# Kernel tuning notes

Measured on AMD Instinct MI355X. Metric: run time of the kernel, lower is better.

## Reference

```python
import jax, jax.numpy as jnp
import numpy as np

N, T, H, D, E, P, R = 50000, 16, 512, 256, 200000, 100000, 3
LN_EPS = 1e-5
BN_EPS = 1e-5


def setup_inputs() -> dict:
    key = jax.random.key(0)
    ks = jax.random.split(key, 32)
    ri = lambda k, shape, hi: jax.random.randint(k, shape, 0, hi)
    rn = lambda k, shape, scale=0.05: (jax.random.normal(k, shape, dtype=jnp.float32) * scale)
    return {
        "node_type_ids": ri(ks[0], (N,), T),
        "src0": ri(ks[1], (E,), N), "dst0": ri(ks[2], (E,), N),
        "src1": ri(ks[3], (E,), N), "dst1": ri(ks[4], (E,), N),
        "src2": ri(ks[5], (E,), N), "dst2": ri(ks[6], (E,), N),
        "pairs": ri(ks[7], (2, P), N),
        "degrees": ri(ks[8], (N,), 100),
        "node_emb": rn(ks[9], (N, H)),
        "type_emb": rn(ks[10], (T, H)),
        "w_loop_in": rn(ks[11], (H, H)),
        "w_rel_in": rn(ks[12], (R, H, H)),
        "w_loop_res": rn(ks[13], (H, H)),
        "w_rel_res": rn(ks[14], (R, H, H)),
        "ln_g": jnp.ones((H,), jnp.float32),
        "ln_b": jnp.zeros((H,), jnp.float32),
        "w_loop_out": rn(ks[15], (H, D)),
        "w_rel_out": rn(ks[16], (R, H, D)),
        "lp_w1": rn(ks[17], (3 * D, D)),
        "lp_b1": jnp.zeros((D,), jnp.float32),
        "bn_g": jnp.ones((D,), jnp.float32),
        "bn_b": jnp.zeros((D,), jnp.float32),
        "bn_mean": jnp.zeros((D,), jnp.float32),
        "bn_var": jnp.ones((D,), jnp.float32),
        "lp_w2": rn(ks[18], (D, 1)),
        "lp_b2": jnp.zeros((1,), jnp.float32),
        "alpha": jnp.float32(0.1),
        "beta": jnp.float32(0.1),
    }


def _rgcn(x, loop_w, rel_w, srcs, dsts):
    # out = x @ W_loop + sum_r (A_r @ x) @ W_r ; A_r unweighted COO -> segment_sum
    out = x @ loop_w
    for r in range(R):
        msg = jax.ops.segment_sum(x[srcs[r]], dsts[r], num_segments=x.shape[0])
        out = out + msg @ rel_w[r]
    return out


def _layernorm(h, g, b):
    mu = h.mean(-1, keepdims=True)
    var = h.var(-1, keepdims=True)
    return (h - mu) * jax.lax.rsqrt(var + LN_EPS) * g + b


def reference(node_type_ids, src0, dst0, src1, dst1, src2, dst2, pairs, degrees,
              node_emb, type_emb, w_loop_in, w_rel_in, w_loop_res, w_rel_res,
              ln_g, ln_b, w_loop_out, w_rel_out, lp_w1, lp_b1, bn_g, bn_b,
              bn_mean, bn_var, lp_w2, lp_b2, alpha, beta):
    srcs = (src0, src1, src2)
    dsts = (dst0, dst1, dst2)
    # encode
    x = node_emb + type_emb[node_type_ids]          # [N, H]
    x = jax.nn.relu(_rgcn(x, w_loop_in, w_rel_in, srcs, dsts))
    h = _rgcn(x, w_loop_res, w_rel_res, srcs, dsts)
    h = jax.nn.relu(_layernorm(h, ln_g, ln_b))      # dropout p=0 -> identity
    x = x + h
    z = _rgcn(x, w_loop_out, w_rel_out, srcs, dsts)  # [N, D]
    # score
    src_z = z[pairs[0]]                              # [P, D]
    dst_z = z[pairs[1]]
    src_deg = jnp.clip(degrees[pairs[0]], 1).astype(jnp.float32)
    dst_deg = jnp.clip(degrees[pairs[1]], 1).astype(jnp.float32)
    feats = jnp.concatenate([src_z, dst_z, src_z * dst_z], axis=-1)  # [P, 3D]
    h1 = jax.nn.relu(feats @ lp_w1 + lp_b1)
    # BatchNorm1d in eval mode: running stats
    h1 = (h1 - bn_mean) * jax.lax.rsqrt(bn_var + BN_EPS) * bn_g + bn_b
    mlp_score = (h1 @ lp_w2 + lp_b2).squeeze(-1)     # [P]
    base = mlp_score - jax.nn.relu(alpha) * jnp.log(src_deg) - jax.nn.relu(beta) * jnp.log(dst_deg)
    return base / (jnp.sqrt(src_deg) * jnp.sqrt(dst_deg) + 1e-8)
```

## Files before the change

kernel.cpp:

```cpp
#include <hip/hip_runtime.h>

typedef __attribute__((ext_vector_type(8))) _Float16 half8;
typedef __attribute__((ext_vector_type(4))) _Float16 half4;
typedef __attribute__((ext_vector_type(4))) float f32x4;

__global__ void k_encode(const float* __restrict__ emb, const float* __restrict__ temb,
                         const int* __restrict__ tids, _Float16* __restrict__ x, int n) {
  int i = blockIdx.x * 256 + threadIdx.x;
  if (i >= n * 64) return;
  int node = i >> 6, c = (i & 63) << 3;
  const float* e = emb + (size_t)node * 512 + c;
  const float* t = temb + (size_t)tids[node] * 512 + c;
  float4 a0 = *(const float4*)e, a1 = *(const float4*)(e + 4);
  float4 b0 = *(const float4*)t, b1 = *(const float4*)(t + 4);
  half8 o;
  o[0] = (_Float16)(a0.x + b0.x); o[1] = (_Float16)(a0.y + b0.y);
  o[2] = (_Float16)(a0.z + b0.z); o[3] = (_Float16)(a0.w + b0.w);
  o[4] = (_Float16)(a1.x + b1.x); o[5] = (_Float16)(a1.y + b1.y);
  o[6] = (_Float16)(a1.z + b1.z); o[7] = (_Float16)(a1.w + b1.w);
  *(half8*)(x + (size_t)node * 512 + c) = o;
}

__global__ void k_zero(int* __restrict__ p, int n) {
  int i = blockIdx.x * 256 + threadIdx.x;
  if (i < n) p[i] = 0;
}

__global__ void k_hist(const int* __restrict__ d0, const int* __restrict__ d1,
                       const int* __restrict__ d2, int* __restrict__ counts, int E, int Np1) {
  int e = blockIdx.x * 256 + threadIdx.x;
  if (e >= E) return;
  int r = blockIdx.y;
  const int* d = (r == 0) ? d0 : ((r == 1) ? d1 : d2);
  atomicAdd(&counts[r * Np1 + d[e] + 1], 1);
}

__global__ void k_scan(const int* __restrict__ counts, int* __restrict__ rowp, int n) {
  __shared__ int wsum[16];
  int r = blockIdx.x;
  const int* c = counts + (size_t)r * n;
  int* o = rowp + (size_t)r * n;
  int lane = threadIdx.x & 63, w = threadIdx.x >> 6;
  int off = 0;
  for (int base = 0; base < n; base += 1024) {
    int i = base + threadIdx.x;
    int v = (i < n) ? c[i] : 0;
    int sc = v;
    #pragma unroll
    for (int d = 1; d < 64; d <<= 1) {
      int t = __shfl_up(sc, (unsigned)d);
      if (lane >= d) sc += t;
    }
    if (lane == 63) wsum[w] = sc;
    __syncthreads();
    int wo = 0, tot = 0;
    #pragma unroll
    for (int ww = 0; ww < 16; ++ww) {
      int s = wsum[ww];
      if (ww < w) wo += s;
      tot += s;
    }
    if (i < n) o[i] = sc + wo + off;
    off += tot;
    __syncthreads();
  }
}

__global__ void k_copy(const int* __restrict__ a, int* __restrict__ b, int n) {
  int i = blockIdx.x * 256 + threadIdx.x;
  if (i < n) b[i] = a[i];
}

__global__ void k_fill(const int* __restrict__ s0, const int* __restrict__ s1, const int* __restrict__ s2,
                       const int* __restrict__ d0, const int* __restrict__ d1, const int* __restrict__ d2,
                       int* __restrict__ cursor, int* __restrict__ col_src, int E, int Np1) {
  int e = blockIdx.x * 256 + threadIdx.x;
  if (e >= E) return;
  int r = blockIdx.y;
  const int* dp = (r == 0) ? d0 : ((r == 1) ? d1 : d2);
  const int* sp = (r == 0) ? s0 : ((r == 1) ? s1 : s2);
  int pos = atomicAdd(&cursor[r * Np1 + dp[e]], 1);
  if (pos >= 0 && pos < E) col_src[(size_t)r * E + pos] = sp[e];
}

__global__ void k_aggregate(const _Float16* __restrict__ x, _Float16* __restrict__ agg,
                            const int* __restrict__ rowp, const int* __restrict__ col_src,
                            int N, int E) {
  int wid = (blockIdx.x * 256 + threadIdx.x) >> 6;
  int lane = threadIdx.x & 63;
  if (wid >= 3 * N) return;
  int r = wid / N;
  int n = wid - r * N;
  int beg = rowp[r * (N + 1) + n], end = rowp[r * (N + 1) + n + 1];
  const int* cs = col_src + (size_t)r * E;
  float acc[8] = {0, 0, 0, 0, 0, 0, 0, 0};
  for (int e = beg; e < end; ++e) {
    int s = cs[e];
    half8 v = *(const half8*)(x + (size_t)s * 512 + lane * 8);
    #pragma unroll
    for (int j = 0; j < 8; ++j) acc[j] += (float)v[j];
  }
  half8 o;
  #pragma unroll
  for (int j = 0; j < 8; ++j) o[j] = (_Float16)acc[j];
  *(half8*)(agg + (size_t)n * 1536 + r * 512 + lane * 8) = o;
}

__global__ void k_transpose(const float* __restrict__ Bl, const float* __restrict__ Br,
                            _Float16* __restrict__ Bt, int No, int K) {
  __shared__ float tile[64][65];
  int k0 = blockIdx.x * 64, n0 = blockIdx.y * 64;
  int nl = threadIdx.x & 63, kb = threadIdx.x >> 6;
  #pragma unroll
  for (int i = 0; i < 16; ++i) {
    int kl = kb + i * 4;
    int krow = k0 + kl;
    float v = (krow < 512) ? Bl[(size_t)krow * No + n0 + nl]
                           : Br[(size_t)(krow - 512) * No + n0 + nl];
    tile[kl][nl] = v;
  }
  __syncthreads();
  int kl = threadIdx.x & 63, nb = threadIdx.x >> 6;
  #pragma unroll
  for (int i = 0; i < 16; ++i) {
    int n2 = nb + i * 4;
    Bt[(size_t)(n0 + n2) * K + k0 + kl] = (_Float16)tile[kl][n2];
  }
}

#define LSTR 40

__global__ __launch_bounds__(256) void k_gemm_rgcn(
    const _Float16* __restrict__ Ain, const _Float16* __restrict__ Aagg,
    const _Float16* __restrict__ Bt, _Float16* __restrict__ C,
    int M, int Ncols, int K, int relu) {
  __shared__ __align__(16) _Float16 As[128 * LSTR];
  __shared__ __align__(16) _Float16 Bs[128 * LSTR];
  int tid = threadIdx.x;
  int bm0 = blockIdx.x * 128, bn0 = blockIdx.y * 128;
  int lane = tid & 63, wv = tid >> 6;
  int wm = wv & 1, wn = wv >> 1;
  int l16 = lane & 15, quad = lane >> 4;
  int srow = tid >> 1, scs = (tid & 1) * 16;
  int agr = bm0 + srow; if (agr >= M) agr = M - 1;
  int bgn = bn0 + srow;

  f32x4 acc[4][4];
  #pragma unroll
  for (int i = 0; i < 4; ++i)
    #pragma unroll
    for (int j = 0; j < 4; ++j) acc[i][j] = (f32x4){0.f, 0.f, 0.f, 0.f};

  for (int k0 = 0; k0 < K; k0 += 32) {
    __syncthreads();
    {
      const _Float16* src = (k0 < 512)
          ? Ain + (size_t)agr * 512 + k0 + scs
          : Aagg + (size_t)agr * 1536 + (k0 - 512) + scs;
      *(uint4*)&As[srow * LSTR + scs] = *(const uint4*)src;
      *(uint4*)&As[srow * LSTR + scs + 8] = *(const uint4*)(src + 8);
    }
    {
      const _Float16* src = Bt + (size_t)bgn * K + k0 + scs;
      *(uint4*)&Bs[srow * LSTR + scs] = *(const uint4*)src;
      *(uint4*)&Bs[srow * LSTR + scs + 8] = *(const uint4*)(src + 8);
    }
    __syncthreads();
    half8 af[4], bf[4];
    #pragma unroll
    for (int i = 0; i < 4; ++i)
      af[i] = *(const half8*)&As[(wm * 64 + i * 16 + l16) * LSTR + quad * 8];
    #pragma unroll
    for (int j = 0; j < 4; ++j)
      bf[j] = *(const half8*)&Bs[(wn * 64 + j * 16 + l16) * LSTR + quad * 8];
    #pragma unroll
    for (int i = 0; i < 4; ++i)
      #pragma unroll
      for (int j = 0; j < 4; ++j)
        acc[i][j] = __builtin_amdgcn_mfma_f32_16x16x32_f16(af[i], bf[j], acc[i][j], 0, 0, 0);
  }

  #pragma unroll
  for (int i = 0; i < 4; ++i)
    #pragma unroll
    for (int j = 0; j < 4; ++j)
      #pragma unroll
      for (int rg = 0; rg < 4; ++rg) {
        int row = bm0 + wm * 64 + i * 16 + quad * 4 + rg;
        int col = bn0 + wn * 64 + j * 16 + l16;
        if (row < M) {
          float v = acc[i][j][rg];
          if (relu) v = fmaxf(v, 0.f);
          C[(size_t)row * Ncols + col] = (_Float16)v;
        }
      }
}

__global__ __launch_bounds__(256) void k_gemm_link(
    const _Float16* __restrict__ z, const int* __restrict__ pairs,
    const _Float16* __restrict__ Bt,
    const float* __restrict__ b1, const float* __restrict__ bng, const float* __restrict__ bnb,
    const float* __restrict__ bnm, const float* __restrict__ bnv,
    _Float16* __restrict__ h1, int P, int K) {
  __shared__ __align__(16) _Float16 As[128 * LSTR];
  __shared__ __align__(16) _Float16 Bs[128 * LSTR];
  int tid = threadIdx.x;
  int bm0 = blockIdx.x * 128, bn0 = blockIdx.y * 128;
  int lane = tid & 63, wv = tid >> 6;
  int wm = wv & 1, wn = wv >> 1;
  int l16 = lane & 15, quad = lane >> 4;
  int srow = tid >> 1, scs = (tid & 1) * 16;
  int p = bm0 + srow; if (p >= P) p = P - 1;
  int sp = pairs[p], dp = pairs[P + p];
  const _Float16* zs = z + (size_t)sp * 256;
  const _Float16* zd = z + (size_t)dp * 256;
  int bgn = bn0 + srow;

  f32x4 acc[4][4];
  #pragma unroll
  for (int i = 0; i < 4; ++i)
    #pragma unroll
    for (int j = 0; j < 4; ++j) acc[i][j] = (f32x4){0.f, 0.f, 0.f, 0.f};

  for (int k0 = 0; k0 < K; k0 += 32) {
    __syncthreads();
    int seg = k0 >> 8;
    int kk = (k0 & 255) + scs;
    __attribute__((aligned(16))) _Float16 tmp[16];
    if (seg == 0) {
      *(uint4*)tmp = *(const uint4*)(zs + kk);
      *(uint4*)(tmp + 8) = *(const uint4*)(zs + kk + 8);
    } else if (seg == 1) {
      *(uint4*)tmp = *(const uint4*)(zd + kk);
      *(uint4*)(tmp + 8) = *(const uint4*)(zd + kk + 8);
    } else {
      half8 u0 = *(const half8*)(zs + kk), u1 = *(const half8*)(zs + kk + 8);
      half8 v0 = *(const half8*)(zd + kk), v1 = *(const half8*)(zd + kk + 8);
      #pragma unroll
      for (int j = 0; j < 8; ++j) {
        tmp[j] = (_Float16)((float)u0[j] * (float)v0[j]);
        tmp[j + 8] = (_Float16)((float)u1[j] * (float)v1[j]);
      }
    }
    *(uint4*)&As[srow * LSTR + scs] = *(const uint4*)tmp;
    *(uint4*)&As[srow * LSTR + scs + 8] = *(const uint4*)(tmp + 8);
    {
      const _Float16* src = Bt + (size_t)bgn * K + k0 + scs;
      *(uint4*)&Bs[srow * LSTR + scs] = *(const uint4*)src;
      *(uint4*)&Bs[srow * LSTR + scs + 8] = *(const uint4*)(src + 8);
    }
    __syncthreads();
    half8 af[4], bf[4];
    #pragma unroll
    for (int i = 0; i < 4; ++i)
      af[i] = *(const half8*)&As[(wm * 64 + i * 16 + l16) * LSTR + quad * 8];
    #pragma unroll
    for (int j = 0; j < 4; ++j)
      bf[j] = *(const half8*)&Bs[(wn * 64 + j * 16 + l16) * LSTR + quad * 8];
    #pragma unroll
    for (int i = 0; i < 4; ++i)
      #pragma unroll
      for (int j = 0; j < 4; ++j)
        acc[i][j] = __builtin_amdgcn_mfma_f32_16x16x32_f16(af[i], bf[j], acc[i][j], 0, 0, 0);
  }

  #pragma unroll
  for (int i = 0; i < 4; ++i)
    #pragma unroll
    for (int j = 0; j < 4; ++j) {
      int col = bn0 + wn * 64 + j * 16 + l16;
      float bb1 = b1[col], m = bnm[col], rs = rsqrtf(bnv[col] + 1e-5f);
      float gg = bng[col], bb = bnb[col];
      #pragma unroll
      for (int rg = 0; rg < 4; ++rg) {
        int row = bm0 + wm * 64 + i * 16 + quad * 4 + rg;
        if (row < P) {
          float v = fmaxf(acc[i][j][rg] + bb1, 0.f);
          v = (v - m) * rs * gg + bb;
          h1[(size_t)row * 256 + col] = (_Float16)v;
        }
      }
    }
}

__global__ void k_ln_res(const _Float16* __restrict__ h, const _Float16* __restrict__ x1,
                         const float* __restrict__ g, const float* __restrict__ b,
                         _Float16* __restrict__ out, int N) {
  int wid = (blockIdx.x * 256 + threadIdx.x) >> 6;
  int lane = threadIdx.x & 63;
  if (wid >= N) return;
  int c = lane * 8;
  half8 hv = *(const half8*)(h + (size_t)wid * 512 + c);
  float hf[8];
  float s = 0.f, sq = 0.f;
  #pragma unroll
  for (int j = 0; j < 8; ++j) {
    hf[j] = (float)hv[j];
    s += hf[j];
    sq += hf[j] * hf[j];
  }
  #pragma unroll
  for (int off = 32; off; off >>= 1) {
    s += __shfl_down(s, (unsigned)off);
    sq += __shfl_down(sq, (unsigned)off);
  }
  s = __shfl(s, 0); sq = __shfl(sq, 0);
  float mu = s * (1.f / 512.f);
  float var = sq * (1.f / 512.f) - mu * mu;
  float rs = rsqrtf(var + 1e-5f);
  float4 g0 = *(const float4*)(g + c), g1 = *(const float4*)(g + c + 4);
  float4 b0 = *(const float4*)(b + c), b1 = *(const float4*)(b + c + 4);
  float gf[8] = {g0.x, g0.y, g0.z, g0.w, g1.x, g1.y, g1.z, g1.w};
  float bf[8] = {b0.x, b0.y, b0.z, b0.w, b1.x, b1.y, b1.z, b1.w};
  half8 xv = *(const half8*)(x1 + (size_t)wid * 512 + c);
  half8 o;
  #pragma unroll
  for (int j = 0; j < 8; ++j) {
    float xw = (float)xv[j];
    o[j] = (_Float16)(xw + fmaxf((hf[j] - mu) * rs * gf[j] + bf[j], 0.f));
  }
  *(half8*)(out + (size_t)wid * 512 + c) = o;
}

__global__ void k_score(const _Float16* __restrict__ h1, const float* __restrict__ w2,
                        const float* __restrict__ b2, const int* __restrict__ pairs,
                        const int* __restrict__ degrees, const float* __restrict__ alpha,
                        const float* __restrict__ beta, float* __restrict__ out, int P) {
  int wid = (blockIdx.x * 256 + threadIdx.x) >> 6;
  int lane = threadIdx.x & 63;
  if (wid >= P) return;
  int c = lane * 4;
  half4 hv = *(const half4*)(h1 + (size_t)wid * 256 + c);
  float4 wv = *(const float4*)(w2 + c);
  float s = (float)hv[0] * wv.x + (float)hv[1] * wv.y + (float)hv[2] * wv.z + (float)hv[3] * wv.w;
  #pragma unroll
  for (int off = 32; off; off >>= 1) s += __shfl_down(s, (unsigned)off);
  if (lane == 0) {
    int sp = pairs[wid], dp = pairs[P + wid];
    float sd = (float)max(degrees[sp], 1);
    float dd = (float)max(degrees[dp], 1);
    float base = s + b2[0] - fmaxf(alpha[0], 0.f) * logf(sd) - fmaxf(beta[0], 0.f) * logf(dd);
    out[wid] = base / (sqrtf(sd) * sqrtf(dd) + 1e-8f);
  }
}

extern "C" void kernel_launch(void* const* d_in, const int* in_sizes, int n_in,
                              void* d_out, int out_size, void* d_ws, size_t ws_size,
                              hipStream_t stream) {
  const int N = 50000, E = 200000, P = 100000;
  const int Np1 = N + 1;
  const int* node_type = (const int*)d_in[0];
  const int* src0 = (const int*)d_in[1]; const int* dst0 = (const int*)d_in[2];
  const int* src1 = (const int*)d_in[3]; const int* dst1 = (const int*)d_in[4];
  const int* src2 = (const int*)d_in[5]; const int* dst2 = (const int*)d_in[6];
  const int* pairs = (const int*)d_in[7];
  const int* degrees = (const int*)d_in[8];
  const float* node_emb = (const float*)d_in[9];
  const float* type_emb = (const float*)d_in[10];
  const float* w_loop_in = (const float*)d_in[11];
  const float* w_rel_in = (const float*)d_in[12];
  const float* w_loop_res = (const float*)d_in[13];
  const float* w_rel_res = (const float*)d_in[14];
  const float* ln_g = (const float*)d_in[15];
  const float* ln_b = (const float*)d_in[16];
  const float* w_loop_out = (const float*)d_in[17];
  const float* w_rel_out = (const float*)d_in[18];
  const float* lp_w1 = (const float*)d_in[19];
  const float* lp_b1 = (const float*)d_in[20];
  const float* bn_g = (const float*)d_in[21];
  const float* bn_b = (const float*)d_in[22];
  const float* bn_mean = (const float*)d_in[23];
  const float* bn_var = (const float*)d_in[24];
  const float* lp_w2 = (const float*)d_in[25];
  const float* lp_b2 = (const float*)d_in[26];
  const float* alpha = (const float*)d_in[27];
  const float* beta = (const float*)d_in[28];
  float* out = (float*)d_out;

  char* ws = (char*)d_ws;
  size_t off = 0;
  auto alloc = [&](size_t bytes) {
    void* p = ws + off;
    off = (off + bytes + 255) & ~(size_t)255;
    return p;
  };
  _Float16* xb0 = (_Float16*)alloc((size_t)N * 512 * 2);
  _Float16* xb1 = (_Float16*)alloc((size_t)N * 512 * 2);
  _Float16* agg = (_Float16*)alloc((size_t)N * 1536 * 2);
  _Float16* Bt = (_Float16*)alloc((size_t)512 * 2048 * 2);
  int* counts = (int*)alloc((size_t)3 * Np1 * 4);
  int* rowp = (int*)alloc((size_t)3 * Np1 * 4);
  int* cursor = (int*)alloc((size_t)3 * Np1 * 4);
  int* col_src = (int*)alloc((size_t)3 * E * 4);
  if (off > ws_size) return;

  _Float16* z = xb1;
  _Float16* h1 = agg;

  k_zero<<<(3 * Np1 + 255) / 256, 256, 0, stream>>>(counts, 3 * Np1);
  dim3 gE((E + 255) / 256, 3);
  k_hist<<<gE, 256, 0, stream>>>(dst0, dst1, dst2, counts, E, Np1);
  k_scan<<<3, 1024, 0, stream>>>(counts, rowp, Np1);
  k_copy<<<(3 * Np1 + 255) / 256, 256, 0, stream>>>(rowp, cursor, 3 * Np1);
  k_fill<<<gE, 256, 0, stream>>>(src0, src1, src2, dst0, dst1, dst2, cursor, col_src, E, Np1);

  k_encode<<<(N * 64 + 255) / 256, 256, 0, stream>>>(node_emb, type_emb, node_type, xb0, N);

  int aggBlocks = (3 * N + 3) / 4;
  dim3 g1((N + 127) / 128, 4);
  dim3 g3((N + 127) / 128, 2);

  k_aggregate<<<aggBlocks, 256, 0, stream>>>(xb0, agg, rowp, col_src, N, E);
  k_transpose<<<dim3(32, 8), 256, 0, stream>>>(w_loop_in, w_rel_in, Bt, 512, 2048);
  k_gemm_rgcn<<<g1, 256, 0, stream>>>(xb0, agg, Bt, xb1, N, 512, 2048, 1);

  k_aggregate<<<aggBlocks, 256, 0, stream>>>(xb1, agg, rowp, col_src, N, E);
  k_transpose<<<dim3(32, 8), 256, 0, stream>>>(w_loop_res, w_rel_res, Bt, 512, 2048);
  k_gemm_rgcn<<<g1, 256, 0, stream>>>(xb1, agg, Bt, xb0, N, 512, 2048, 0);

  k_ln_res<<<(N + 3) / 4, 256, 0, stream>>>(xb0, xb1, ln_g, ln_b, xb0, N);

  k_aggregate<<<aggBlocks, 256, 0, stream>>>(xb0, agg, rowp, col_src, N, E);
  k_transpose<<<dim3(32, 4), 256, 0, stream>>>(w_loop_out, w_rel_out, Bt, 256, 2048);
  k_gemm_rgcn<<<g3, 256, 0, stream>>>(xb0, agg, Bt, z, N, 256, 2048, 0);

  k_transpose<<<dim3(12, 4), 256, 0, stream>>>(lp_w1, lp_w1 + 512 * 256, Bt, 256, 768);
  dim3 gl((P + 127) / 128, 2);
  k_gemm_link<<<gl, 256, 0, stream>>>(z, pairs, Bt, lp_b1, bn_g, bn_b, bn_mean, bn_var, h1, P, 768);

  k_score<<<(P + 3) / 4, 256, 0, stream>>>(h1, lp_w2, lp_b2, pairs, degrees, alpha, beta, out, P);
}
```

Before: 1.294 ms.

## Use direct global-to-LDS loads in RGCN GEMM and swap grid axes

The RGCN GEMM now stages A and B tiles with global_load_lds 16-byte loads straight into LDS instead of going through registers. The LDS padding (stride 40) is dropped to a dense stride of 32 to match the per-wave contiguous layout those loads write. Separately, the grid axes of both GEMMs are swapped so consecutive blocks share the same A row-block across N tiles, which should improve L2 reuse of activations. The unpadded LDS layout may add bank conflicts on the fragment reads.

```diff
diff --git a/kernel.cpp b/kernel.cpp
--- a/kernel.cpp
+++ b/kernel.cpp
@@ -3,6 +3,11 @@
 typedef __attribute__((ext_vector_type(8))) _Float16 half8;
 typedef __attribute__((ext_vector_type(4))) _Float16 half4;
 typedef __attribute__((ext_vector_type(4))) float f32x4;
+
+static __device__ __forceinline__ void gload16(const void* g, void* l) {
+  __builtin_amdgcn_global_load_lds((const __attribute__((address_space(1))) void*)g,
+                                   (__attribute__((address_space(3))) void*)l, 16, 0, 0);
+}
 
 __global__ void k_encode(const float* __restrict__ emb, const float* __restrict__ temb,
                          const int* __restrict__ tids, _Float16* __restrict__ x, int n) {
@@ -128,22 +133,32 @@
   }
 }
 
-#define LSTR 40
-
 __global__ __launch_bounds__(256) void k_gemm_rgcn(
     const _Float16* __restrict__ Ain, const _Float16* __restrict__ Aagg,
     const _Float16* __restrict__ Bt, _Float16* __restrict__ C,
     int M, int Ncols, int K, int relu) {
-  __shared__ __align__(16) _Float16 As[128 * LSTR];
-  __shared__ __align__(16) _Float16 Bs[128 * LSTR];
+  __shared__ __align__(16) _Float16 As[128 * 32];
+  __shared__ __align__(16) _Float16 Bs[128 * 32];
   int tid = threadIdx.x;
-  int bm0 = blockIdx.x * 128, bn0 = blockIdx.y * 128;
+  int bn0 = blockIdx.x * 128, bm0 = blockIdx.y * 128;
   int lane = tid & 63, wv = tid >> 6;
   int wm = wv & 1, wn = wv >> 1;
   int l16 = lane & 15, quad = lane >> 4;
-  int srow = tid >> 1, scs = (tid & 1) * 16;
-  int agr = bm0 + srow; if (agr >= M) agr = M - 1;
-  int bgn = bn0 + srow;
+
+  int rl = wv * 16 + (lane >> 2);
+  int kq = (lane & 3) * 8;
+  int ra0 = bm0 + rl;       if (ra0 >= M) ra0 = M - 1;
+  int ra1 = bm0 + 64 + rl;  if (ra1 >= M) ra1 = M - 1;
+  int rb0 = bn0 + rl, rb1 = bn0 + 64 + rl;
+
+  const _Float16* pa0 = Ain + (size_t)ra0 * 512 + kq;
+  const _Float16* pa1 = Ain + (size_t)ra1 * 512 + kq;
+  const _Float16* pb0 = Bt + (size_t)rb0 * K + kq;
+  const _Float16* pb1 = Bt + (size_t)rb1 * K + kq;
+  _Float16* la0 = &As[(wv * 16) * 32];
+  _Float16* la1 = &As[(64 + wv * 16) * 32];
+  _Float16* lb0 = &Bs[(wv * 16) * 32];
+  _Float16* lb1 = &Bs[(64 + wv * 16) * 32];
 
   f32x4 acc[4][4];
   #pragma unroll
@@ -152,32 +167,29 @@
     for (int j = 0; j < 4; ++j) acc[i][j] = (f32x4){0.f, 0.f, 0.f, 0.f};
 
   for (int k0 = 0; k0 < K; k0 += 32) {
-    __syncthreads();
-    {
-      const _Float16* src = (k0 < 512)
-          ? Ain + (size_t)agr * 512 + k0 + scs
-          : Aagg + (size_t)agr * 1536 + (k0 - 512) + scs;
-      *(uint4*)&As[srow * LSTR + scs] = *(const uint4*)src;
-      *(uint4*)&As[srow * LSTR + scs + 8] = *(const uint4*)(src + 8);
-    }
-    {
-      const _Float16* src = Bt + (size_t)bgn * K + k0 + scs;
-      *(uint4*)&Bs[srow * LSTR + scs] = *(const uint4*)src;
-      *(uint4*)&Bs[srow * LSTR + scs + 8] = *(const uint4*)(src + 8);
-    }
+    if (k0 == 512) {
+      pa0 = Aagg + (size_t)ra0 * 1536 + kq;
+      pa1 = Aagg + (size_t)ra1 * 1536 + kq;
+    }
+    __syncthreads();
+    gload16(pa0, la0);
+    gload16(pa1, la1);
+    gload16(pb0, lb0);
+    gload16(pb1, lb1);
     __syncthreads();
     half8 af[4], bf[4];
     #pragma unroll
     for (int i = 0; i < 4; ++i)
-      af[i] = *(const half8*)&As[(wm * 64 + i * 16 + l16) * LSTR + quad * 8];
+      af[i] = *(const half8*)&As[(wm * 64 + i * 16 + l16) * 32 + quad * 8];
     #pragma unroll
     for (int j = 0; j < 4; ++j)
-      bf[j] = *(const half8*)&Bs[(wn * 64 + j * 16 + l16) * LSTR + quad * 8];
+      bf[j] = *(const half8*)&Bs[(wn * 64 + j * 16 + l16) * 32 + quad * 8];
     #pragma unroll
     for (int i = 0; i < 4; ++i)
       #pragma unroll
       for (int j = 0; j < 4; ++j)
         acc[i][j] = __builtin_amdgcn_mfma_f32_16x16x32_f16(af[i], bf[j], acc[i][j], 0, 0, 0);
+    pa0 += 32; pa1 += 32; pb0 += 32; pb1 += 32;
   }
 
   #pragma unroll
@@ -196,6 +208,8 @@
       }
 }
 
+#define LSTR 40
+
 __global__ __launch_bounds__(256) void k_gemm_link(
     const _Float16* __restrict__ z, const int* __restrict__ pairs,
     const _Float16* __restrict__ Bt,
@@ -205,7 +219,7 @@
   __shared__ __align__(16) _Float16 As[128 * LSTR];
   __shared__ __align__(16) _Float16 Bs[128 * LSTR];
   int tid = threadIdx.x;
-  int bm0 = blockIdx.x * 128, bn0 = blockIdx.y * 128;
+  int bn0 = blockIdx.x * 128, bm0 = blockIdx.y * 128;
   int lane = tid & 63, wv = tid >> 6;
   int wm = wv & 1, wn = wv >> 1;
   int l16 = lane & 15, quad = lane >> 4;
@@ -407,8 +421,8 @@
   k_encode<<<(N * 64 + 255) / 256, 256, 0, stream>>>(node_emb, type_emb, node_type, xb0, N);
 
   int aggBlocks = (3 * N + 3) / 4;
-  dim3 g1((N + 127) / 128, 4);
-  dim3 g3((N + 127) / 128, 2);
+  dim3 g1(4, (N + 127) / 128);
+  dim3 g3(2, (N + 127) / 128);
 
   k_aggregate<<<aggBlocks, 256, 0, stream>>>(xb0, agg, rowp, col_src, N, E);
   k_transpose<<<dim3(32, 8), 256, 0, stream>>>(w_loop_in, w_rel_in, Bt, 512, 2048);
@@ -425,7 +439,7 @@
   k_gemm_rgcn<<<g3, 256, 0, stream>>>(xb0, agg, Bt, z, N, 256, 2048, 0);
 
   k_transpose<<<dim3(12, 4), 256, 0, stream>>>(lp_w1, lp_w1 + 512 * 256, Bt, 256, 768);
-  dim3 gl((P + 127) / 128, 2);
+  dim3 gl(2, (P + 127) / 128);
   k_gemm_link<<<gl, 256, 0, stream>>>(z, pairs, Bt, lp_b1, bn_g, bn_b, bn_mean, bn_var, h1, P, 768);
 
   k_score<<<(P + 3) / 4, 256, 0, stream>>>(h1, lp_w2, lp_b2, pairs, degrees, alpha, beta, out, P);
```

After: 1.263 ms. 2.4% less time.
